# Kernel optimization log

Measured on AMD Instinct MI355X. Metric: run time of the kernel, lower is better.

The kernel has to match this reference:

```python
import jax, jax.numpy as jnp
import numpy as np

N, E = 50000, 800000
IN, HID, OUT = 128, 128, 64
H, ED = 4, 3
D = HID // H  # per-head dim = 32


def _w(key, shape):
    fan_in = shape[-1]
    return jax.random.normal(key, shape, dtype=jnp.float32) / np.sqrt(fan_in)


def setup_inputs() -> dict:
    key = jax.random.key(0)
    ks = jax.random.split(key, 32)
    inp = {
        "x": jax.random.normal(ks[0], (N, IN), dtype=jnp.float32),
        "edge_index": jax.random.randint(ks[1], (2, E), 0, N, dtype=jnp.int32),
        "edge_attr": jax.random.normal(ks[2], (E, ED), dtype=jnp.float32),
        # layer 1 TransformerConv (bias=False)
        "Wq1": _w(ks[3], (HID, IN)), "Wk1": _w(ks[4], (HID, IN)),
        "Wv1": _w(ks[5], (HID, IN)), "We1": _w(ks[6], (HID, ED)),
        "Ws1": _w(ks[7], (HID, IN)),
        # layer 1 MLP [HID,HID,HID]
        "M1a": _w(ks[8], (HID, HID)), "b1a": jnp.zeros((HID,), jnp.float32),
        "M1b": _w(ks[9], (HID, HID)), "b1b": jnp.zeros((HID,), jnp.float32),
        # layer 2 TransformerConv
        "Wq2": _w(ks[10], (HID, HID)), "Wk2": _w(ks[11], (HID, HID)),
        "Wv2": _w(ks[12], (HID, HID)), "We2": _w(ks[13], (HID, ED)),
        "Ws2": _w(ks[14], (HID, HID)),
        # layer 2 MLP
        "M2a": _w(ks[15], (HID, HID)), "b2a": jnp.zeros((HID,), jnp.float32),
        "M2b": _w(ks[16], (HID, HID)), "b2b": jnp.zeros((HID,), jnp.float32),
        # final MLP [HID,HID,OUT], plain_last=False
        "Wf1": _w(ks[17], (HID, HID)), "bf1": jnp.zeros((HID,), jnp.float32),
        "Wf2": _w(ks[18], (OUT, HID)), "bf2": jnp.zeros((OUT,), jnp.float32),
    }
    return inp


def _gelu(x):
    return jax.nn.gelu(x, approximate=True)


def _transformer_conv(x, src, dst, edge_attr, Wq, Wk, Wv, We, Ws, n_nodes):
    # PyG TransformerConv: x_j = x[src] (message source), x_i = x[dst] (target)
    q = (x @ Wq.T).reshape(n_nodes, H, D)
    e = (edge_attr @ We.T).reshape(-1, H, D)              # [E,H,D]
    k = (x @ Wk.T).reshape(n_nodes, H, D)[src] + e        # [E,H,D]
    v = (x @ Wv.T).reshape(n_nodes, H, D)[src] + e        # [E,H,D]
    alpha = jnp.einsum("ehd,ehd->eh", q[dst], k) / jnp.float32(np.sqrt(D))
    # segment softmax over incoming edges of each target node
    m = jax.ops.segment_max(alpha, dst, num_segments=n_nodes)  # [N,H]
    m = jnp.where(jnp.isfinite(m), m, 0.0)
    p = jnp.exp(alpha - m[dst])
    s = jax.ops.segment_sum(p, dst, num_segments=n_nodes)      # [N,H]
    a = p / jnp.maximum(s[dst], 1e-16)                         # [E,H]
    out = jax.ops.segment_sum(a[:, :, None] * v, dst, num_segments=n_nodes)
    out = out.reshape(n_nodes, H * D)
    # root_weight=True (default): skip connection through lin_skip (no bias)
    return out + x @ Ws.T


def _mlp2(x, Wa, ba, Wb, bb):
    # PyG MLP with plain_last=False: act after every linear, norm=None
    h = _gelu(x @ Wa.T + ba)
    return _gelu(h @ Wb.T + bb)


def reference(x, edge_index, edge_attr,
              Wq1, Wk1, Wv1, We1, Ws1, M1a, b1a, M1b, b1b,
              Wq2, Wk2, Wv2, We2, Ws2, M2a, b2a, M2b, b2b,
              Wf1, bf1, Wf2, bf2):
    n_nodes = x.shape[0]
    src, dst = edge_index[0], edge_index[1]
    h = _transformer_conv(x, src, dst, edge_attr, Wq1, Wk1, Wv1, We1, Ws1, n_nodes)
    h = h + _mlp2(h, M1a, b1a, M1b, b1b)
    h = _transformer_conv(h, src, dst, edge_attr, Wq2, Wk2, Wv2, We2, Ws2, n_nodes)
    h = h + _mlp2(h, M2a, b2a, M2b, b2b)
    return _mlp2(h, Wf1, bf1, Wf2, bf2)
```

## Files before the change

### kernel.cpp

```cpp
#include <hip/hip_runtime.h>
#include <hip/hip_bf16.h>
#include <math.h>

#define NN 50000
#define NE 800000
#define NPAD 50048
#define NB_SCAN 196

typedef unsigned short u16;
typedef unsigned int u32;
typedef __attribute__((ext_vector_type(8))) short short8;
typedef __attribute__((ext_vector_type(4))) float float4v;

__device__ __forceinline__ float us2f(u16 u) { return __uint_as_float(((unsigned)u) << 16); }
__device__ __forceinline__ float blo(u32 u) { return __uint_as_float(u << 16); }
__device__ __forceinline__ float bhi(u32 u) { return __uint_as_float(u & 0xffff0000u); }
__device__ __forceinline__ u16 f2us(float f) {
    unsigned x = __float_as_uint(f);
    return (u16)((x + 0x7FFFu + ((x >> 16) & 1u)) >> 16);
}
__device__ __forceinline__ float gelu_f(float x) {
    float p = x * x;
    float t = x * fmaf(p, 0.0713548162726f, 1.5957691216057308f);
    float e = __expf(-t);
    return x * __builtin_amdgcn_rcpf(1.0f + e);
}
__device__ __forceinline__ void lds_fence() {
    asm volatile("s_waitcnt lgkmcnt(0)" ::: "memory");
}

__device__ __forceinline__ float4v mfma4p(const u16* __restrict__ WP, int tile, int l,
                                          short8 a0, short8 a1, short8 a2, short8 a3) {
    const short8* wp = (const short8*)WP + (size_t)tile * 256 + l;
    short8 b0 = wp[0], b1 = wp[64], b2 = wp[128], b3 = wp[192];
    float4v acc = {0.f, 0.f, 0.f, 0.f};
    acc = __builtin_amdgcn_mfma_f32_16x16x32_bf16(a0, b0, acc, 0, 0, 0);
    acc = __builtin_amdgcn_mfma_f32_16x16x32_bf16(a1, b1, acc, 0, 0, 0);
    acc = __builtin_amdgcn_mfma_f32_16x16x32_bf16(a2, b2, acc, 0, 0, 0);
    acc = __builtin_amdgcn_mfma_f32_16x16x32_bf16(a3, b3, acc, 0, 0, 0);
    return acc;
}


__global__ void k_hist(const int* __restrict__ dstv, int* __restrict__ deg) {
    int e = blockIdx.x * blockDim.x + threadIdx.x;
    if (e < NE) atomicAdd(&deg[dstv[e]], 1);
}

__global__ __launch_bounds__(256) void k_scan1(const int* __restrict__ deg,
                                               int* __restrict__ rowstart,
                                               int* __restrict__ bsum) {
    __shared__ int wtot[4];
    int i = blockIdx.x * 256 + threadIdx.x;
    int lane = threadIdx.x & 63, w = threadIdx.x >> 6;
    int v = (i < NN) ? deg[i] : 0;
    int incl = v;
#pragma unroll
    for (int d = 1; d < 64; d <<= 1) {
        int tv = __shfl_up(incl, d);
        if (lane >= d) incl += tv;
    }
    if (lane == 63) wtot[w] = incl;
    __syncthreads();
    if (threadIdx.x == 0) {
        int s = 0;
#pragma unroll
        for (int j = 0; j < 4; ++j) { int t = wtot[j]; wtot[j] = s; s += t; }
        bsum[blockIdx.x] = s;
    }
    __syncthreads();
    if (i < NN) rowstart[i] = incl - v + wtot[w];
}

__global__ __launch_bounds__(256) void k_scan2(int* __restrict__ bsum) {
    __shared__ int wtot[4];
    int t = threadIdx.x;
    int lane = t & 63, w = t >> 6;
    int v = (t < NB_SCAN) ? bsum[t] : 0;
    int incl = v;
#pragma unroll
    for (int d = 1; d < 64; d <<= 1) {
        int tv = __shfl_up(incl, d);
        if (lane >= d) incl += tv;
    }
    if (lane == 63) wtot[w] = incl;
    __syncthreads();
    if (t == 0) {
        int s = 0;
#pragma unroll
        for (int j = 0; j < 4; ++j) { int tt = wtot[j]; wtot[j] = s; s += tt; }
    }
    __syncthreads();
    if (t < NB_SCAN) bsum[t] = incl - v + wtot[w];
}

__global__ void k_scan3(const int* __restrict__ bsum, int* __restrict__ rowstart,
                        int* __restrict__ cursor) {
    int i = blockIdx.x * 256 + threadIdx.x;
    if (i < NN) {
        int v = rowstart[i] + bsum[blockIdx.x];
        rowstart[i] = v;
        cursor[i] = v;
    }
    if (i == 0) rowstart[NN] = NE;
}

__global__ void k_scatter(const int* __restrict__ srcv, const int* __restrict__ dstv,
                          const float* __restrict__ eattr, int* __restrict__ cursor,
                          int4* __restrict__ rec) {
    int e = blockIdx.x * blockDim.x + threadIdx.x;
    if (e >= NE) return;
    int dst = dstv[e];
    int pos = atomicAdd(&cursor[dst], 1);
    int4 r;
    r.x = srcv[e];
    r.y = __float_as_int(eattr[e * 3 + 0]);
    r.z = __float_as_int(eattr[e * 3 + 1]);
    r.w = __float_as_int(eattr[e * 3 + 2]);
    rec[pos] = r;
}


struct CvtEnt { const float* s; u16* d; int n; };
struct CvtTab { CvtEnt e[14]; };
__global__ void k_cvt_w(CvtTab tab) {
    CvtEnt E = tab.e[blockIdx.x >> 3];
    int chunk = blockIdx.x & 7;
    int per = E.n >> 3;
    int lo = chunk * per, hi = lo + per;
    for (int o = lo + threadIdx.x; o < hi; o += blockDim.x) {
        int tile = o >> 11;
        int q = (o >> 9) & 3;
        int l = (o >> 3) & 63;
        int j = o & 7;
        int row = tile * 16 + (l & 15);
        int col = q * 32 + (l >> 4) * 8 + j;
        E.d[o] = f2us(E.s[row * 128 + col]);
    }
}


__device__ __forceinline__ void stage_plain(u16* buf, int kb, int m, int tt, float4v acc) {
#pragma unroll
    for (int r = 0; r < 4; ++r) buf[(kb * 4 + r) * 136 + tt * 16 + m] = f2us(acc[r]);
}
__device__ __forceinline__ void store128(const u16* buf, u16* dst, int r0w, int coff, int l) {
#pragma unroll
    for (int it = 0; it < 4; ++it) {
        int j = it * 64 + l;
        int row = j >> 4, col = (j & 15) * 8;
        *(uint4*)(dst + (size_t)(r0w + row) * 512 + coff + col) = *(const uint4*)&buf[row * 136 + col];
    }
}
__device__ __forceinline__ void read_frags(const u16* buf, int m, int kb,
                                           short8& f0, short8& f1, short8& f2, short8& f3) {
    const u16* p = buf + m * 136 + kb * 8;
    f0 = *(const short8*)(p);
    f1 = *(const short8*)(p + 32);
    f2 = *(const short8*)(p + 64);
    f3 = *(const short8*)(p + 96);
}


__global__ __launch_bounds__(256, 4) void k_qkvs1(const float* __restrict__ Ain,
                                                  const u16* __restrict__ W,
                                                  u16* __restrict__ QKVS) {
    __shared__ u16 tile[4][16 * 136];
    int tid = threadIdx.x;
    int l = tid & 63, w = tid >> 6, m = l & 15, kb = l >> 4;
    int r0w = blockIdx.x * 64 + w * 16;
    u16* my = tile[w];

    short8 a0, a1, a2, a3;
    {
        const float* ap = Ain + (size_t)(r0w + m) * 128;
        bool ok = (r0w + m) < NN;
        short8* dsts[4] = {&a0, &a1, &a2, &a3};
#pragma unroll
        for (int i = 0; i < 4; ++i) {
            short8 r;
            if (ok) {
                const float* p = ap + (kb + i * 4) * 8;
                float4 f0 = *(const float4*)p;
                float4 f1 = *(const float4*)(p + 4);
                r[0]=(short)f2us(f0.x); r[1]=(short)f2us(f0.y); r[2]=(short)f2us(f0.z); r[3]=(short)f2us(f0.w);
                r[4]=(short)f2us(f1.x); r[5]=(short)f2us(f1.y); r[6]=(short)f2us(f1.z); r[7]=(short)f2us(f1.w);
            } else {
#pragma unroll
                for (int j = 0; j < 8; ++j) r[j] = 0;
            }
            *dsts[i] = r;
        }
    }

#pragma unroll
    for (int tt = 0; tt < 8; ++tt) stage_plain(my, kb, m, tt, mfma4p(W, tt, l, a0, a1, a2, a3));
    lds_fence();
    store128(my, QKVS, r0w, 0, l);
    lds_fence();
#pragma unroll
    for (int tt = 0; tt < 4; ++tt) {
        float4v acc = mfma4p(W, 8 + tt, l, a0, a1, a2, a3);
        int c = tt * 32 + 8 * (m >> 2) + (m & 3);
#pragma unroll
        for (int r = 0; r < 4; ++r) my[(kb * 4 + r) * 136 + c] = f2us(acc[r]);
    }
#pragma unroll
    for (int tt = 0; tt < 4; ++tt) {
        float4v acc = mfma4p(W, 16 + tt, l, a0, a1, a2, a3);
        int c = tt * 32 + 8 * (m >> 2) + (m & 3) + 4;
#pragma unroll
        for (int r = 0; r < 4; ++r) my[(kb * 4 + r) * 136 + c] = f2us(acc[r]);
    }
    lds_fence();
    store128(my, QKVS, r0w, 128, l);
    lds_fence();
#pragma unroll
    for (int tt = 0; tt < 4; ++tt) {
        float4v acc = mfma4p(W, 12 + tt, l, a0, a1, a2, a3);
        int c = tt * 32 + 8 * (m >> 2) + (m & 3);
#pragma unroll
        for (int r = 0; r < 4; ++r) my[(kb * 4 + r) * 136 + c] = f2us(acc[r]);
    }
#pragma unroll
    for (int tt = 0; tt < 4; ++tt) {
        float4v acc = mfma4p(W, 20 + tt, l, a0, a1, a2, a3);
        int c = tt * 32 + 8 * (m >> 2) + (m & 3) + 4;
#pragma unroll
        for (int r = 0; r < 4; ++r) my[(kb * 4 + r) * 136 + c] = f2us(acc[r]);
    }
    lds_fence();
    store128(my, QKVS, r0w, 256, l);
    lds_fence();
#pragma unroll
    for (int tt = 0; tt < 8; ++tt) stage_plain(my, kb, m, tt, mfma4p(W, 24 + tt, l, a0, a1, a2, a3));
    lds_fence();
    store128(my, QKVS, r0w, 384, l);
}


__global__ __launch_bounds__(256, 4) void k_mlp_qkvs(const u16* __restrict__ Ain,
                                                     const u16* __restrict__ Wm,
                                                     const float* __restrict__ bias1,
                                                     const float* __restrict__ bias2,
                                                     const u16* __restrict__ Wq,
                                                     u16* __restrict__ QKVS) {
    __shared__ u16 shb[4][16 * 136];
    __shared__ u16 t1b[4][16 * 136];
    int tid = threadIdx.x;
    int l = tid & 63, w = tid >> 6, m = l & 15, kb = l >> 4;
    int r0w = blockIdx.x * 64 + w * 16;
    u16* sh = shb[w];
    u16* t1 = t1b[w];

    const short8* arow = (const short8*)(Ain + (size_t)(r0w + m) * 128);
    short8 a0 = arow[kb], a1 = arow[kb + 4], a2 = arow[kb + 8], a3 = arow[kb + 12];
    {
        u16* p = sh + m * 136 + kb * 8;
        *(short8*)(p) = a0;
        *(short8*)(p + 32) = a1;
        *(short8*)(p + 64) = a2;
        *(short8*)(p + 96) = a3;
    }
#pragma unroll
    for (int tt = 0; tt < 8; ++tt) {
        float4v acc = mfma4p(Wm, tt, l, a0, a1, a2, a3);
        float bv = bias1[tt * 16 + m];
#pragma unroll
        for (int r = 0; r < 4; ++r)
            t1[(kb * 4 + r) * 136 + tt * 16 + m] = f2us(gelu_f(acc[r] + bv));
    }
    lds_fence();
    short8 c0, c1, c2, c3;
    read_frags(t1, m, kb, c0, c1, c2, c3);
#pragma unroll
    for (int tt = 0; tt < 8; ++tt) {
        float4v acc = mfma4p(Wm + 16384, tt, l, c0, c1, c2, c3);
        float bv = bias2[tt * 16 + m];
#pragma unroll
        for (int r = 0; r < 4; ++r) {
            int idx = (kb * 4 + r) * 136 + tt * 16 + m;
            sh[idx] = f2us(gelu_f(acc[r] + bv) + us2f(sh[idx]));
        }
    }
    lds_fence();
    short8 h0, h1, h2, h3;
    read_frags(sh, m, kb, h0, h1, h2, h3);

#pragma unroll
    for (int tt = 0; tt < 8; ++tt) stage_plain(t1, kb, m, tt, mfma4p(Wq, tt, l, h0, h1, h2, h3));
    lds_fence();
    store128(t1, QKVS, r0w, 0, l);
    lds_fence();
#pragma unroll
    for (int tt = 0; tt < 4; ++tt) {
        float4v acc = mfma4p(Wq, 8 + tt, l, h0, h1, h2, h3);
        int c = tt * 32 + 8 * (m >> 2) + (m & 3);
#pragma unroll
        for (int r = 0; r < 4; ++r) t1[(kb * 4 + r) * 136 + c] = f2us(acc[r]);
    }
#pragma unroll
    for (int tt = 0; tt < 4; ++tt) {
        float4v acc = mfma4p(Wq, 16 + tt, l, h0, h1, h2, h3);
        int c = tt * 32 + 8 * (m >> 2) + (m & 3) + 4;
#pragma unroll
        for (int r = 0; r < 4; ++r) t1[(kb * 4 + r) * 136 + c] = f2us(acc[r]);
    }
    lds_fence();
    store128(t1, QKVS, r0w, 128, l);
    lds_fence();
#pragma unroll
    for (int tt = 0; tt < 4; ++tt) {
        float4v acc = mfma4p(Wq, 12 + tt, l, h0, h1, h2, h3);
        int c = tt * 32 + 8 * (m >> 2) + (m & 3);
#pragma unroll
        for (int r = 0; r < 4; ++r) t1[(kb * 4 + r) * 136 + c] = f2us(acc[r]);
    }
#pragma unroll
    for (int tt = 0; tt < 4; ++tt) {
        float4v acc = mfma4p(Wq, 20 + tt, l, h0, h1, h2, h3);
        int c = tt * 32 + 8 * (m >> 2) + (m & 3) + 4;
#pragma unroll
        for (int r = 0; r < 4; ++r) t1[(kb * 4 + r) * 136 + c] = f2us(acc[r]);
    }
    lds_fence();
    store128(t1, QKVS, r0w, 256, l);
    lds_fence();
#pragma unroll
    for (int tt = 0; tt < 8; ++tt) stage_plain(t1, kb, m, tt, mfma4p(Wq, 24 + tt, l, h0, h1, h2, h3));
    lds_fence();
    store128(t1, QKVS, r0w, 384, l);
}


__global__ __launch_bounds__(256, 4) void k_mlp_final(const u16* __restrict__ Ain,
                                                      const u16* __restrict__ Wm,
                                                      const float* __restrict__ bias1,
                                                      const float* __restrict__ bias2,
                                                      const u16* __restrict__ Wf,
                                                      const float* __restrict__ bf1,
                                                      const float* __restrict__ bf2,
                                                      float* __restrict__ outp) {
    __shared__ u16 shb[4][16 * 136];
    __shared__ u16 t1b[4][16 * 136];
    int tid = threadIdx.x;
    int l = tid & 63, w = tid >> 6, m = l & 15, kb = l >> 4;
    int r0w = blockIdx.x * 64 + w * 16;
    u16* sh = shb[w];
    u16* t1 = t1b[w];

    const short8* arow = (const short8*)(Ain + (size_t)(r0w + m) * 128);
    short8 a0 = arow[kb], a1 = arow[kb + 4], a2 = arow[kb + 8], a3 = arow[kb + 12];
    {
        u16* p = sh + m * 136 + kb * 8;
        *(short8*)(p) = a0;
        *(short8*)(p + 32) = a1;
        *(short8*)(p + 64) = a2;
        *(short8*)(p + 96) = a3;
    }
#pragma unroll
    for (int tt = 0; tt < 8; ++tt) {
        float4v acc = mfma4p(Wm, tt, l, a0, a1, a2, a3);
        float bv = bias1[tt * 16 + m];
#pragma unroll
        for (int r = 0; r < 4; ++r)
            t1[(kb * 4 + r) * 136 + tt * 16 + m] = f2us(gelu_f(acc[r] + bv));
    }
    lds_fence();
    short8 c0, c1, c2, c3;
    read_frags(t1, m, kb, c0, c1, c2, c3);
#pragma unroll
    for (int tt = 0; tt < 8; ++tt) {
        float4v acc = mfma4p(Wm + 16384, tt, l, c0, c1, c2, c3);
        float bv = bias2[tt * 16 + m];
#pragma unroll
        for (int r = 0; r < 4; ++r) {
            int idx = (kb * 4 + r) * 136 + tt * 16 + m;
            sh[idx] = f2us(gelu_f(acc[r] + bv) + us2f(sh[idx]));
        }
    }
    lds_fence();
    short8 h0, h1, h2, h3;
    read_frags(sh, m, kb, h0, h1, h2, h3);
#pragma unroll
    for (int tt = 0; tt < 8; ++tt) {
        float4v acc = mfma4p(Wf, tt, l, h0, h1, h2, h3);
        float bv = bf1[tt * 16 + m];
#pragma unroll
        for (int r = 0; r < 4; ++r)
            t1[(kb * 4 + r) * 136 + tt * 16 + m] = f2us(gelu_f(acc[r] + bv));
    }
    lds_fence();
    short8 f0, f1, f2, f3;
    read_frags(t1, m, kb, f0, f1, f2, f3);
    lds_fence();
#pragma unroll
    for (int tt = 0; tt < 4; ++tt) {
        float4v acc = mfma4p(Wf + 16384, tt, l, f0, f1, f2, f3);
        float bv = bf2[tt * 16 + m];
#pragma unroll
        for (int r = 0; r < 4; ++r)
            t1[(kb * 4 + r) * 136 + tt * 16 + m] = f2us(gelu_f(acc[r] + bv));
    }
    lds_fence();
#pragma unroll
    for (int it = 0; it < 2; ++it) {
        int j = it * 64 + l;
        int row = j >> 3, col = (j & 7) * 8;
        int grow = r0w + row;
        if (grow < NN) {
            uint4 pk = *(const uint4*)&t1[row * 136 + col];
            const u16* pv = (const u16*)&pk;
            float* po = outp + (size_t)grow * 64 + col;
            float4 o0 = {us2f(pv[0]), us2f(pv[1]), us2f(pv[2]), us2f(pv[3])};
            float4 o1 = {us2f(pv[4]), us2f(pv[5]), us2f(pv[6]), us2f(pv[7])};
            *(float4*)po = o0;
            *(float4*)(po + 4) = o1;
        }
    }
}


__global__ __launch_bounds__(256) void k_conv(const int* __restrict__ rowstart,
                                              const int4* __restrict__ rec,
                                              const u16* __restrict__ qkvs,
                                              const float* __restrict__ We,
                                              u16* __restrict__ out) {
    int n = blockIdx.x * 4 + (threadIdx.x >> 6);
    int l = threadIdx.x & 63;
    int half = l >> 5;
    int li = l & 31;
    int c0 = (li >> 3) * 32 + (li & 7) * 4;
    const u16* qrow = qkvs + (size_t)n * 512;
    uint2 qu = *(const uint2*)(qrow + c0);
    float q0 = blo(qu.x), q1 = bhi(qu.x), q2 = blo(qu.y), q3 = bhi(qu.y);
    float w00 = We[c0 * 3 + 0], w01 = We[c0 * 3 + 1], w02 = We[c0 * 3 + 2];
    float w10 = We[c0 * 3 + 3], w11 = We[c0 * 3 + 4], w12 = We[c0 * 3 + 5];
    float w20 = We[c0 * 3 + 6], w21 = We[c0 * 3 + 7], w22 = We[c0 * 3 + 8];
    float w30 = We[c0 * 3 + 9], w31 = We[c0 * 3 + 10], w32 = We[c0 * 3 + 11];
    float g0 = fmaf(q3, w30, fmaf(q2, w20, fmaf(q1, w10, q0 * w00)));
    float g1 = fmaf(q3, w31, fmaf(q2, w21, fmaf(q1, w11, q0 * w01)));
    float g2 = fmaf(q3, w32, fmaf(q2, w22, fmaf(q1, w12, q0 * w02)));
#pragma unroll
    for (int d = 1; d <= 4; d <<= 1) {
        g0 += __shfl_xor(g0, d);
        g1 += __shfl_xor(g1, d);
        g2 += __shfl_xor(g2, d);
    }
    int e0 = rowstart[n], e1 = rowstart[n + 1];
    float ss = 0.f, o0 = 0.f, o1 = 0.f, o2 = 0.f, o3 = 0.f, S0 = 0.f, S1 = 0.f, S2 = 0.f;
    int kvoff = 128 + li * 8;

    auto edge = [&](int4 r, uint4 kv) {
        float part = fmaf(q3, bhi(kv.y), fmaf(q2, blo(kv.y), fmaf(q1, bhi(kv.x), q0 * blo(kv.x))));
        part += __shfl_xor(part, 1);
        part += __shfl_xor(part, 2);
        part += __shfl_xor(part, 4);
        float ea0 = __int_as_float(r.y), ea1 = __int_as_float(r.z), ea2 = __int_as_float(r.w);
        float alpha = fmaf(ea2, g2, fmaf(ea1, g1, fmaf(ea0, g0, part))) * 0.17677669529663687f;
        float p = __expf(fminf(alpha, 80.f));
        o0 = fmaf(p, blo(kv.z), o0);
        o1 = fmaf(p, bhi(kv.z), o1);
        o2 = fmaf(p, blo(kv.w), o2);
        o3 = fmaf(p, bhi(kv.w), o3);
        ss += p;
        S0 = fmaf(p, ea0, S0);
        S1 = fmaf(p, ea1, S1);
        S2 = fmaf(p, ea2, S2);
    };

    int e = e0 + half;
    int cnt = (e < e1) ? ((e1 - e + 1) >> 1) : 0;
    if (cnt & 1) {
        int4 r = rec[e];
        uint4 kv = *(const uint4*)(qkvs + (size_t)r.x * 512 + kvoff);
        edge(r, kv);
        e += 2;
    }
    for (int i = 0; i < (cnt >> 1); ++i, e += 4) {
        int4 ra = rec[e], rb = rec[e + 2];
        uint4 kva = *(const uint4*)(qkvs + (size_t)ra.x * 512 + kvoff);
        uint4 kvb = *(const uint4*)(qkvs + (size_t)rb.x * 512 + kvoff);
        edge(ra, kva);
        edge(rb, kvb);
    }
    o0 += __shfl_xor(o0, 32);
    o1 += __shfl_xor(o1, 32);
    o2 += __shfl_xor(o2, 32);
    o3 += __shfl_xor(o3, 32);
    ss += __shfl_xor(ss, 32);
    S0 += __shfl_xor(S0, 32);
    S1 += __shfl_xor(S1, 32);
    S2 += __shfl_xor(S2, 32);
    if (half == 0) {
        float inv = __builtin_amdgcn_rcpf(fmaxf(ss, 1e-16f));
        o0 = fmaf(w02, S2, fmaf(w01, S1, fmaf(w00, S0, o0)));
        o1 = fmaf(w12, S2, fmaf(w11, S1, fmaf(w10, S0, o1)));
        o2 = fmaf(w22, S2, fmaf(w21, S1, fmaf(w20, S0, o2)));
        o3 = fmaf(w32, S2, fmaf(w31, S1, fmaf(w30, S0, o3)));
        uint2 su = *(const uint2*)(qrow + 384 + c0);
        float r0v = fmaf(o0, inv, blo(su.x));
        float r1v = fmaf(o1, inv, bhi(su.x));
        float r2v = fmaf(o2, inv, blo(su.y));
        float r3v = fmaf(o3, inv, bhi(su.y));
        uint2 ou;
        ou.x = (u32)f2us(r0v) | ((u32)f2us(r1v) << 16);
        ou.y = (u32)f2us(r2v) | ((u32)f2us(r3v) << 16);
        *(uint2*)(out + (size_t)n * 128 + c0) = ou;
    }
}


extern "C" void kernel_launch(void* const* d_in, const int* in_sizes, int n_in,
                              void* d_out, int out_size, void* d_ws, size_t ws_size,
                              hipStream_t stream) {
    const float* x = (const float*)d_in[0];
    const int* ei = (const int*)d_in[1];
    const float* eattr = (const float*)d_in[2];
    const float* Wq1 = (const float*)d_in[3];
    const float* Wk1 = (const float*)d_in[4];
    const float* Wv1 = (const float*)d_in[5];
    const float* We1 = (const float*)d_in[6];
    const float* Ws1 = (const float*)d_in[7];
    const float* M1a = (const float*)d_in[8];
    const float* b1a = (const float*)d_in[9];
    const float* M1b = (const float*)d_in[10];
    const float* b1b = (const float*)d_in[11];
    const float* Wq2 = (const float*)d_in[12];
    const float* Wk2 = (const float*)d_in[13];
    const float* Wv2 = (const float*)d_in[14];
    const float* We2 = (const float*)d_in[15];
    const float* Ws2 = (const float*)d_in[16];
    const float* M2a = (const float*)d_in[17];
    const float* b2a = (const float*)d_in[18];
    const float* M2b = (const float*)d_in[19];
    const float* b2b = (const float*)d_in[20];
    const float* Wf1 = (const float*)d_in[21];
    const float* bf1 = (const float*)d_in[22];
    const float* Wf2 = (const float*)d_in[23];
    const float* bf2 = (const float*)d_in[24];

    char* ws = (char*)d_ws;
    size_t off = 0;
    auto alloc = [&](size_t bytes) -> void* {
        void* p = ws + off;
        off = (off + bytes + 255) & ~(size_t)255;
        return p;
    };
    int* deg = (int*)alloc((size_t)NN * 4);
    int* rowstart = (int*)alloc((size_t)(NN + 1) * 4);
    int* cursor = (int*)alloc((size_t)NN * 4);
    int* bsum = (int*)alloc((size_t)NB_SCAN * 4);
    int4* rec = (int4*)alloc((size_t)NE * 16);
    u16* QKVS = (u16*)alloc((size_t)NPAD * 512 * 2);
    u16* Ha = (u16*)alloc((size_t)NPAD * 128 * 2);
    u16* WB[14];
    const int wsz[14] = {16384, 16384, 16384, 16384, 16384, 16384, 16384,
                         16384, 16384, 16384, 16384, 16384, 16384, 8192};
    for (int i = 0; i < 14; ++i) WB[i] = (u16*)alloc((size_t)wsz[i] * 2);

    const int* srcv = ei;
    const int* dstv = ei + NE;

    hipMemsetAsync(deg, 0, (size_t)NN * 4, stream);
    k_hist<<<(NE + 255) / 256, 256, 0, stream>>>(dstv, deg);
    k_scan1<<<NB_SCAN, 256, 0, stream>>>(deg, rowstart, bsum);
    k_scan2<<<1, 256, 0, stream>>>(bsum);
    k_scan3<<<NB_SCAN, 256, 0, stream>>>(bsum, rowstart, cursor);
    k_scatter<<<(NE + 255) / 256, 256, 0, stream>>>(srcv, dstv, eattr, cursor, rec);

    CvtTab tab;
    const float* wsrc[14] = {Wq1, Wk1, Wv1, Ws1, Wq2, Wk2, Wv2, Ws2,
                             M1a, M1b, M2a, M2b, Wf1, Wf2};
    for (int i = 0; i < 14; ++i) { tab.e[i].s = wsrc[i]; tab.e[i].d = WB[i]; tab.e[i].n = wsz[i]; }
    k_cvt_w<<<112, 256, 0, stream>>>(tab);

    dim3 blk(256);
    dim3 grd(NPAD / 64);
    dim3 gconv(NN / 4);

    k_qkvs1<<<grd, blk, 0, stream>>>(x, WB[0], QKVS);
    k_conv<<<gconv, blk, 0, stream>>>(rowstart, rec, QKVS, We1, Ha);
    k_mlp_qkvs<<<grd, blk, 0, stream>>>(Ha, WB[8], b1a, b1b, WB[4], QKVS);
    k_conv<<<gconv, blk, 0, stream>>>(rowstart, rec, QKVS, We2, Ha);
    k_mlp_final<<<grd, blk, 0, stream>>>(Ha, WB[10], b2a, b2b, WB[12], bf1, bf2, (float*)d_out);
}
```

Before: 408.0 us.

## Split conv wavefront into four edge groups with 8 channels per lane

The per-node attention conv kernel now gives each wavefront four quarter-groups of 16 lanes. Each lane covers 8 channels instead of 4, and the four groups process edges in parallel, where before two halves took alternating edges. This widens the per-lane K/V loads, shortens the dot-product shuffle reduction, and keeps more edge gathers in flight per node. In exchange it adds more accumulator registers, a masked tail loop and a two-step cross-group reduction, and lanes can sit idle on nodes with few edges.

```diff
diff --git a/kernel.cpp b/kernel.cpp
--- a/kernel.cpp
+++ b/kernel.cpp
@@ -428,85 +428,100 @@
                                               u16* __restrict__ out) {
     int n = blockIdx.x * 4 + (threadIdx.x >> 6);
     int l = threadIdx.x & 63;
-    int half = l >> 5;
-    int li = l & 31;
-    int c0 = (li >> 3) * 32 + (li & 7) * 4;
+    int qd = l >> 4;
+    int t = l & 15;
+    int c0 = (t >> 2) * 32 + (t & 3) * 8;
     const u16* qrow = qkvs + (size_t)n * 512;
-    uint2 qu = *(const uint2*)(qrow + c0);
+    uint4 qu = *(const uint4*)(qrow + c0);
     float q0 = blo(qu.x), q1 = bhi(qu.x), q2 = blo(qu.y), q3 = bhi(qu.y);
-    float w00 = We[c0 * 3 + 0], w01 = We[c0 * 3 + 1], w02 = We[c0 * 3 + 2];
-    float w10 = We[c0 * 3 + 3], w11 = We[c0 * 3 + 4], w12 = We[c0 * 3 + 5];
-    float w20 = We[c0 * 3 + 6], w21 = We[c0 * 3 + 7], w22 = We[c0 * 3 + 8];
-    float w30 = We[c0 * 3 + 9], w31 = We[c0 * 3 + 10], w32 = We[c0 * 3 + 11];
-    float g0 = fmaf(q3, w30, fmaf(q2, w20, fmaf(q1, w10, q0 * w00)));
-    float g1 = fmaf(q3, w31, fmaf(q2, w21, fmaf(q1, w11, q0 * w01)));
-    float g2 = fmaf(q3, w32, fmaf(q2, w22, fmaf(q1, w12, q0 * w02)));
-#pragma unroll
-    for (int d = 1; d <= 4; d <<= 1) {
-        g0 += __shfl_xor(g0, d);
-        g1 += __shfl_xor(g1, d);
-        g2 += __shfl_xor(g2, d);
+    float q4 = blo(qu.z), q5 = bhi(qu.z), q6 = blo(qu.w), q7 = bhi(qu.w);
+    float g0 = 0.f, g1 = 0.f, g2 = 0.f;
+    {
+        const float* wp = We + c0 * 3;
+        float qq[8] = {q0, q1, q2, q3, q4, q5, q6, q7};
+#pragma unroll
+        for (int j = 0; j < 8; ++j) {
+            g0 = fmaf(qq[j], wp[j * 3 + 0], g0);
+            g1 = fmaf(qq[j], wp[j * 3 + 1], g1);
+            g2 = fmaf(qq[j], wp[j * 3 + 2], g2);
+        }
+        g0 += __shfl_xor(g0, 1); g1 += __shfl_xor(g1, 1); g2 += __shfl_xor(g2, 1);
+        g0 += __shfl_xor(g0, 2); g1 += __shfl_xor(g1, 2); g2 += __shfl_xor(g2, 2);
     }
     int e0 = rowstart[n], e1 = rowstart[n + 1];
-    float ss = 0.f, o0 = 0.f, o1 = 0.f, o2 = 0.f, o3 = 0.f, S0 = 0.f, S1 = 0.f, S2 = 0.f;
-    int kvoff = 128 + li * 8;
-
-    auto edge = [&](int4 r, uint4 kv) {
-        float part = fmaf(q3, bhi(kv.y), fmaf(q2, blo(kv.y), fmaf(q1, bhi(kv.x), q0 * blo(kv.x))));
+    int cnt = e1 - e0;
+    float ss = 0.f, S0 = 0.f, S1 = 0.f, S2 = 0.f;
+    float o0 = 0.f, o1 = 0.f, o2 = 0.f, o3 = 0.f, o4 = 0.f, o5 = 0.f, o6 = 0.f, o7 = 0.f;
+    const u16* kvbase = qkvs + 128 + t * 16;
+
+    auto edge = [&](int4 r, uint4 ka, uint4 kb, bool valid) {
+        float part = fmaf(q7, bhi(kb.y), fmaf(q6, blo(kb.y),
+                     fmaf(q5, bhi(kb.x), fmaf(q4, blo(kb.x),
+                     fmaf(q3, bhi(ka.y), fmaf(q2, blo(ka.y),
+                     fmaf(q1, bhi(ka.x), q0 * blo(ka.x))))))));
         part += __shfl_xor(part, 1);
         part += __shfl_xor(part, 2);
-        part += __shfl_xor(part, 4);
         float ea0 = __int_as_float(r.y), ea1 = __int_as_float(r.z), ea2 = __int_as_float(r.w);
         float alpha = fmaf(ea2, g2, fmaf(ea1, g1, fmaf(ea0, g0, part))) * 0.17677669529663687f;
-        float p = __expf(fminf(alpha, 80.f));
-        o0 = fmaf(p, blo(kv.z), o0);
-        o1 = fmaf(p, bhi(kv.z), o1);
-        o2 = fmaf(p, blo(kv.w), o2);
-        o3 = fmaf(p, bhi(kv.w), o3);
+        float p = valid ? __expf(fminf(alpha, 80.f)) : 0.f;
+        o0 = fmaf(p, blo(ka.z), o0);
+        o1 = fmaf(p, bhi(ka.z), o1);
+        o2 = fmaf(p, blo(ka.w), o2);
+        o3 = fmaf(p, bhi(ka.w), o3);
+        o4 = fmaf(p, blo(kb.z), o4);
+        o5 = fmaf(p, bhi(kb.z), o5);
+        o6 = fmaf(p, blo(kb.w), o6);
+        o7 = fmaf(p, bhi(kb.w), o7);
         ss += p;
         S0 = fmaf(p, ea0, S0);
         S1 = fmaf(p, ea1, S1);
         S2 = fmaf(p, ea2, S2);
     };
 
-    int e = e0 + half;
-    int cnt = (e < e1) ? ((e1 - e + 1) >> 1) : 0;
-    if (cnt & 1) {
-        int4 r = rec[e];
-        uint4 kv = *(const uint4*)(qkvs + (size_t)r.x * 512 + kvoff);
-        edge(r, kv);
-        e += 2;
-    }
-    for (int i = 0; i < (cnt >> 1); ++i, e += 4) {
-        int4 ra = rec[e], rb = rec[e + 2];
-        uint4 kva = *(const uint4*)(qkvs + (size_t)ra.x * 512 + kvoff);
-        uint4 kvb = *(const uint4*)(qkvs + (size_t)rb.x * 512 + kvoff);
-        edge(ra, kva);
-        edge(rb, kvb);
-    }
-    o0 += __shfl_xor(o0, 32);
-    o1 += __shfl_xor(o1, 32);
-    o2 += __shfl_xor(o2, 32);
-    o3 += __shfl_xor(o3, 32);
-    ss += __shfl_xor(ss, 32);
-    S0 += __shfl_xor(S0, 32);
-    S1 += __shfl_xor(S1, 32);
-    S2 += __shfl_xor(S2, 32);
-    if (half == 0) {
+    int i = 0;
+    for (; i + 8 <= cnt; i += 8) {
+        int4 ra = rec[e0 + i + qd];
+        int4 rb = rec[e0 + i + 4 + qd];
+        const uint4* pa = (const uint4*)(kvbase + (size_t)ra.x * 512);
+        const uint4* pb = (const uint4*)(kvbase + (size_t)rb.x * 512);
+        uint4 ka0 = pa[0], ka1 = pa[1];
+        uint4 kb0 = pb[0], kb1 = pb[1];
+        edge(ra, ka0, ka1, true);
+        edge(rb, kb0, kb1, true);
+    }
+    for (; i < cnt; i += 4) {
+        int ia = i + qd;
+        int4 ra = rec[e0 + min(ia, cnt - 1)];
+        const uint4* pa = (const uint4*)(kvbase + (size_t)ra.x * 512);
+        uint4 ka0 = pa[0], ka1 = pa[1];
+        edge(ra, ka0, ka1, ia < cnt);
+    }
+
+#define CMB2(x) x += __shfl_xor(x, 16); x += __shfl_xor(x, 32)
+    CMB2(o0); CMB2(o1); CMB2(o2); CMB2(o3);
+    CMB2(o4); CMB2(o5); CMB2(o6); CMB2(o7);
+    CMB2(ss); CMB2(S0); CMB2(S1); CMB2(S2);
+#undef CMB2
+
+    if (qd == 0) {
         float inv = __builtin_amdgcn_rcpf(fmaxf(ss, 1e-16f));
-        o0 = fmaf(w02, S2, fmaf(w01, S1, fmaf(w00, S0, o0)));
-        o1 = fmaf(w12, S2, fmaf(w11, S1, fmaf(w10, S0, o1)));
-        o2 = fmaf(w22, S2, fmaf(w21, S1, fmaf(w20, S0, o2)));
-        o3 = fmaf(w32, S2, fmaf(w31, S1, fmaf(w30, S0, o3)));
-        uint2 su = *(const uint2*)(qrow + 384 + c0);
-        float r0v = fmaf(o0, inv, blo(su.x));
-        float r1v = fmaf(o1, inv, bhi(su.x));
-        float r2v = fmaf(o2, inv, blo(su.y));
-        float r3v = fmaf(o3, inv, bhi(su.y));
-        uint2 ou;
-        ou.x = (u32)f2us(r0v) | ((u32)f2us(r1v) << 16);
-        ou.y = (u32)f2us(r2v) | ((u32)f2us(r3v) << 16);
-        *(uint2*)(out + (size_t)n * 128 + c0) = ou;
+        const float* wp = We + c0 * 3;
+        float oo[8] = {o0, o1, o2, o3, o4, o5, o6, o7};
+#pragma unroll
+        for (int j = 0; j < 8; ++j)
+            oo[j] = fmaf(wp[j * 3 + 2], S2, fmaf(wp[j * 3 + 1], S1, fmaf(wp[j * 3 + 0], S0, oo[j])));
+        uint4 su = *(const uint4*)(qrow + 384 + c0);
+        float sv[8] = {blo(su.x), bhi(su.x), blo(su.y), bhi(su.y),
+                       blo(su.z), bhi(su.z), blo(su.w), bhi(su.w)};
+        float rv[8];
+#pragma unroll
+        for (int j = 0; j < 8; ++j) rv[j] = fmaf(oo[j], inv, sv[j]);
+        uint4 ou;
+        ou.x = (u32)f2us(rv[0]) | ((u32)f2us(rv[1]) << 16);
+        ou.y = (u32)f2us(rv[2]) | ((u32)f2us(rv[3]) << 16);
+        ou.z = (u32)f2us(rv[4]) | ((u32)f2us(rv[5]) << 16);
+        ou.w = (u32)f2us(rv[6]) | ((u32)f2us(rv[7]) << 16);
+        *(uint4*)(out + (size_t)n * 128 + c0) = ou;
     }
 }
 
```

Result: no change. 412.5 us (+1.1%).
